# Performance work log

Hardware: AMD Instinct MI355X
Metric: run time of the kernel (lower is better)

## Reference

```python
import jax, jax.numpy as jnp
import numpy as np

EPS = 1e-7

def fake_quant(x, bits):
    """Per-tensor affine fake-quantization (dnn-gating TorchRoundToBits),
    matching torch.fake_quantize_per_tensor_affine with dynamic range."""
    fp_max = jax.lax.stop_gradient(jnp.max(x))
    fp_min = jax.lax.stop_gradient(jnp.min(x))
    qmax = float(2 ** bits - 1)
    qmin = 0.0
    scale = (fp_max - fp_min) / (qmax - qmin) + EPS
    zero_point = jnp.trunc(qmin - fp_min / scale)  # int() cast in torch truncates
    q = jnp.round(x / scale + zero_point)
    qc = jnp.clip(q, qmin, qmax)
    return (qc - zero_point) * scale

def conv2d(x, w, stride=1, padding=1):
    return jax.lax.conv_general_dilated(
        x, w,
        window_strides=(stride, stride),
        padding=[(padding, padding), (padding, padding)],
        dimension_numbers=('NCHW', 'OIHW', 'NCHW'))

def setup_inputs() -> dict:
    key = jax.random.key(0)
    k1, k2 = jax.random.split(key)
    x = jax.random.normal(k1, (32, 256, 56, 56), dtype=jnp.float32)
    # kaiming-like init for a 3x3 conv with 256 in-channels
    fan_in = 256 * 3 * 3
    weight = jax.random.normal(k2, (256, 256, 3, 3), dtype=jnp.float32) / np.sqrt(fan_in)
    return {"x": x, "weight": weight}

def reference(x, weight):
    WBITS, ABITS, PGABITS = 8, 8, 4
    TH = 0.99
    w_q = fake_quant(weight, WBITS)          # quantized weights (shared by both convs)
    msb_in = fake_quant(x, PGABITS)          # low-precision (MSB) input
    msb_out = conv2d(msb_in, w_q)            # [32,256,56,56] prediction pass
    lsb_in = fake_quant(x, ABITS) - msb_in   # residual (LSB) input
    lsb_out = conv2d(lsb_in, w_q)            # high-precision correction pass
    mask = (jax.nn.sigmoid(msb_out) > TH).astype(msb_out.dtype)
    return msb_out + mask * lsb_out
```

## Files before the change

kernel.cpp:

```cpp
#include <hip/hip_runtime.h>
#include <stdint.h>
#include <stddef.h>

typedef int v4i  __attribute__((ext_vector_type(4)));
typedef int v16i __attribute__((ext_vector_type(16)));

struct QParams {
  float s4, z4, s8, z8, sw, zw;
  float s4sw, s8sw;
  int dw;
};

__global__ void k_minmax2(const float4* __restrict__ x, int nx4,
                          const float4* __restrict__ w, int nw4,
                          float2* __restrict__ mmX, float2* __restrict__ mmW) {
  const float4* p; int n4; float2* slot; int base; int nblk;
  if (blockIdx.x < 1024) { p = x; n4 = nx4; slot = mmX + blockIdx.x;          base = blockIdx.x;        nblk = 1024; }
  else                   { p = w; n4 = nw4; slot = mmW + (blockIdx.x - 1024); base = blockIdx.x - 1024; nblk = 64; }
  float lmin = 3.4e38f, lmax = -3.4e38f;
  for (int i = base * blockDim.x + threadIdx.x; i < n4; i += nblk * blockDim.x) {
    float4 v = p[i];
    lmin = fminf(lmin, fminf(fminf(v.x, v.y), fminf(v.z, v.w)));
    lmax = fmaxf(lmax, fmaxf(fmaxf(v.x, v.y), fmaxf(v.z, v.w)));
  }
  for (int off = 32; off; off >>= 1) {
    lmin = fminf(lmin, __shfl_down(lmin, off, 64));
    lmax = fmaxf(lmax, __shfl_down(lmax, off, 64));
  }
  __shared__ float smin[4], smax[4];
  int w2 = threadIdx.x >> 6, lane = threadIdx.x & 63;
  if (lane == 0) { smin[w2] = lmin; smax[w2] = lmax; }
  __syncthreads();
  if (threadIdx.x == 0) {
    float2 r;
    r.x = fminf(fminf(smin[0], smin[1]), fminf(smin[2], smin[3]));
    r.y = fmaxf(fmaxf(smax[0], smax[1]), fmaxf(smax[2], smax[3]));
    *slot = r;
  }
}

__device__ __forceinline__ void quant2(float v, float s4, float z4, float s8, float z8,
                                       char& o4, char& o8) {
  float q4 = rintf(__fdiv_rn(v, s4) + z4);
  q4 = fminf(fmaxf(q4, 0.0f), 15.0f);
  o4 = (char)(int)(q4 - z4);
  float q8 = rintf(__fdiv_rn(v, s8) + z8);
  q8 = fminf(fmaxf(q8, 0.0f), 255.0f);
  int t8 = (int)(q8 - z8);
  o8 = (char)max(-128, min(127, t8));
}

__global__ void k_quant(const float4* __restrict__ x4, const float* __restrict__ wt,
                        const float2* __restrict__ mmX, const float2* __restrict__ mmW,
                        char* __restrict__ A4, char* __restrict__ A8,
                        int* __restrict__ CS4, int* __restrict__ CS8,
                        char* __restrict__ Wc,
                        QParams* __restrict__ prm, unsigned* __restrict__ zp) {
  __shared__ char sm4[56 * 260];
  __shared__ char sm8[56 * 260];
  __shared__ int cp4[56][4], cp8[56][4];
  __shared__ float s_red[4][4];
  __shared__ QParams sq;
  int tid = threadIdx.x;

  {
    float xmn = 3.4e38f, xmx = -3.4e38f, wmn = 3.4e38f, wmx = -3.4e38f;
#pragma unroll
    for (int i = 0; i < 4; ++i) {
      float2 v = mmX[i * 256 + tid];
      xmn = fminf(xmn, v.x); xmx = fmaxf(xmx, v.y);
    }
    if (tid < 64) { float2 v = mmW[tid]; wmn = v.x; wmx = v.y; }
    for (int off = 32; off; off >>= 1) {
      xmn = fminf(xmn, __shfl_down(xmn, off, 64));
      xmx = fmaxf(xmx, __shfl_down(xmx, off, 64));
      wmn = fminf(wmn, __shfl_down(wmn, off, 64));
      wmx = fmaxf(wmx, __shfl_down(wmx, off, 64));
    }
    int wv = tid >> 6, ln = tid & 63;
    if (ln == 0) { s_red[wv][0] = xmn; s_red[wv][1] = xmx; s_red[wv][2] = wmn; s_red[wv][3] = wmx; }
    __syncthreads();
    if (tid == 0) {
      float xmin = fminf(fminf(s_red[0][0], s_red[1][0]), fminf(s_red[2][0], s_red[3][0]));
      float xmax = fmaxf(fmaxf(s_red[0][1], s_red[1][1]), fmaxf(s_red[2][1], s_red[3][1]));
      float wmin = fminf(fminf(s_red[0][2], s_red[1][2]), fminf(s_red[2][2], s_red[3][2]));
      float wmax = fmaxf(fmaxf(s_red[0][3], s_red[1][3]), fmaxf(s_red[2][3], s_red[3][3]));
      float s4 = (xmax - xmin) / 15.0f + 1e-7f;
      sq.s4 = s4; sq.z4 = truncf(0.0f - xmin / s4);
      float s8 = (xmax - xmin) / 255.0f + 1e-7f;
      sq.s8 = s8; sq.z8 = truncf(0.0f - xmin / s8);
      float sw = (wmax - wmin) / 255.0f + 1e-7f;
      sq.sw = sw; sq.zw = truncf(0.0f - wmin / sw);
      sq.s4sw = s4 * sw; sq.s8sw = s8 * sw;
      sq.dw = 128 - (int)sq.zw;
    }
    __syncthreads();
  }

  if (blockIdx.x >= 1792) {
    int b = blockIdx.x - 1792;
    float sw = sq.sw, zw = sq.zw;
    char* smw = sm4;
    const float* src = wt + (size_t)b * 2304;
#pragma unroll
    for (int j = 0; j < 9; ++j) {
      int o = j * 256 + tid;
      float qf = rintf(__fdiv_rn(src[o], sw) + zw);
      qf = fminf(fmaxf(qf, 0.0f), 255.0f);
      int c = o / 9, jj = o - c * 9;
      smw[jj * 256 + c] = (char)((int)qf - 128);
    }
    __syncthreads();
    if (tid < 64) {
#pragma unroll
      for (int j = 0; j < 9; ++j)
        *(unsigned*)(Wc + (size_t)j * 65536 + b * 256 + tid * 4) =
            *(const unsigned*)(smw + j * 256 + tid * 4);
    }
    if (blockIdx.x == 1792) {
      if (tid < 128) zp[tid] = 0u;
      if (tid == 0) *prm = sq;
    }
    return;
  }

  int bx = blockIdx.x;
  int n = bx / 56, y = bx % 56;
  float s4 = sq.s4, z4 = sq.z4, s8 = sq.s8, z8 = sq.z8;
  const float4* xrow = x4 + (size_t)n * 200704 + y * 14;
#pragma unroll 2
  for (int it = 0; it < 14; ++it) {
    int idx = it * 256 + tid;
    int c = idx / 14, xq = idx - c * 14;
    float4 v = xrow[(size_t)c * 784 + xq];
    int b = (xq * 4) * 260 + c;
    char a0, b0; quant2(v.x, s4, z4, s8, z8, a0, b0);
    char a1, b1; quant2(v.y, s4, z4, s8, z8, a1, b1);
    char a2, b2; quant2(v.z, s4, z4, s8, z8, a2, b2);
    char a3, b3; quant2(v.w, s4, z4, s8, z8, a3, b3);
    sm4[b] = a0; sm4[b + 260] = a1; sm4[b + 520] = a2; sm4[b + 780] = a3;
    sm8[b] = b0; sm8[b + 260] = b1; sm8[b + 520] = b2; sm8[b + 780] = b3;
  }
  __syncthreads();
  if (tid < 224) {
    int xc = tid >> 2, qq = tid & 3;
    const unsigned* r4 = (const unsigned*)(sm4 + xc * 260 + qq * 64);
    const unsigned* r8 = (const unsigned*)(sm8 + xc * 260 + qq * 64);
    int a = 0, b = 0;
#pragma unroll
    for (int cw = 0; cw < 16; ++cw) {
      unsigned u = r4[cw], v = r8[cw];
      a += (int)(signed char)(u) + (int)(signed char)(u >> 8)
         + (int)(signed char)(u >> 16) + (int)(signed char)(u >> 24);
      b += (int)(signed char)(v) + (int)(signed char)(v >> 8)
         + (int)(signed char)(v >> 16) + (int)(signed char)(v >> 24);
    }
    cp4[xc][qq] = a; cp8[xc][qq] = b;
  }
  __syncthreads();
  int pixbase = n * 3136 + y * 56;
  if (tid < 56) {
    CS4[pixbase + tid] = cp4[tid][0] + cp4[tid][1] + cp4[tid][2] + cp4[tid][3];
    CS8[pixbase + tid] = cp8[tid][0] + cp8[tid][1] + cp8[tid][2] + cp8[tid][3];
  }
  unsigned* A4w = (unsigned*)A4;
  unsigned* A8w = (unsigned*)A8;
#pragma unroll 2
  for (int it = 0; it < 14; ++it) {
    int idx = it * 256 + tid;
    int xc = idx >> 6, wd = idx & 63;
    size_t o = (size_t)(pixbase + xc) * 64 + wd;
    A4w[o] = *(const unsigned*)(sm4 + xc * 260 + wd * 4);
    A8w[o] = *(const unsigned*)(sm8 + xc * 260 + wd * 4);
  }
}

__global__ void k_wsum(const int* __restrict__ CS4, const int* __restrict__ CS8,
                       int* __restrict__ S4, int* __restrict__ S8) {
  int p = blockIdx.x * 256 + threadIdx.x;
  if (p >= 100352) return;
  int rem = p % 3136;
  int y = rem / 56, xc = rem % 56;
  int a = 0, b = 0;
#pragma unroll
  for (int dy = -1; dy <= 1; ++dy) {
    if ((unsigned)(y + dy) >= 56u) continue;
#pragma unroll
    for (int dx = -1; dx <= 1; ++dx) {
      if ((unsigned)(xc + dx) >= 56u) continue;
      int qq = p + dy * 56 + dx;
      a += CS4[qq]; b += CS8[qq];
    }
  }
  S4[p] = a; S8[p] = b;
}

#define GLD16(gp, lp)                                                         \
  __builtin_amdgcn_global_load_lds((const __attribute__((address_space(1))) void*)(gp), \
                                   (__attribute__((address_space(3))) void*)(lp), 16, 0, 0)

__device__ __forceinline__ float pg_merge(int a4v, int a8v, float fs4, float fs8) {
  float msb = fs4 * (float)a4v;
  float c8  = fs8 * (float)a8v;
  float lsb = c8 - msb;
  float sig = 1.0f / (1.0f + expf(-msb));
  return msb + (sig > 0.99f ? lsb : 0.0f);
}

struct StagePtrs {
  const char* aBase0; const char* aBase1;
  const char* a8Base0; const char* a8Base1;
  const char* bBase0; const char* bBase1;
  const char* zp0;
  unsigned vm0, vm1;
};

__device__ __forceinline__ void issue_stage(int s, const StagePtrs& P,
                                            char* dA4, char* dA8, char* dB) {
  int win = s >> 2;
  int cs = (s & 3) << 6;
  int dy = win / 3 - 1;
  int dx = win - (dy + 1) * 3 - 1;
  int doff = (dy * 56 + dx) * 256 + cs;
  bool ok0 = (P.vm0 >> win) & 1;
  bool ok1 = (P.vm1 >> win) & 1;
  const char* g40 = ok0 ? P.aBase0 + doff : P.zp0;
  const char* g41 = ok1 ? P.aBase1 + doff : P.zp0;
  const char* g80 = ok0 ? P.a8Base0 + doff : P.zp0;
  const char* g81 = ok1 ? P.a8Base1 + doff : P.zp0;
  const char* gB0 = P.bBase0 + win * 65536 + cs;
  const char* gB1 = P.bBase1 + win * 65536 + cs;
  if (s >= 36) { gB0 = P.zp0; gB1 = P.zp0; }
  GLD16(g40, dA4);       GLD16(g41, dA4 + 1024);
  GLD16(g80, dA8);       GLD16(g81, dA8 + 1024);
  GLD16(gB0, dB);        GLD16(gB1, dB + 1024);
}

__global__ __launch_bounds__(256, 2) void k_conv(
    const char* __restrict__ A4, const char* __restrict__ A8,
    const char* __restrict__ Wc,
    const int* __restrict__ S4, const int* __restrict__ S8,
    const QParams* __restrict__ q, const char* __restrict__ zpage,
    float* __restrict__ out) {
  __shared__ char smA4[2][8192], smA8[2][8192], smB[2][8192];
  const size_t ASZ = 25690112;
  int tid = threadIdx.x;
  int w = tid >> 6, lane = tid & 63;

  int bid = blockIdx.x;
  int swz = (bid & 7) * 196 + (bid >> 3);
  int m0 = (swz >> 1) * 128;
  int n0 = (swz & 1) * 128;
  int wm = w >> 1, wn = w & 1;

  int chunk = lane & 3;
  int r0 = (w << 5) + (lane >> 2);
  int r1 = r0 + 16;
  int cg0 = chunk ^ ((r0 >> 1) & 3);
  int cg1 = chunk ^ ((r1 >> 1) & 3);
  int p0 = m0 + r0, p1 = m0 + r1;
  int rem0 = p0 % 3136, rem1 = p1 % 3136;
  int y0 = rem0 / 56, x0 = rem0 % 56;
  int y1 = rem1 / 56, x1 = rem1 % 56;

  StagePtrs P;
  P.aBase0 = A4 + (size_t)p0 * 256 + cg0 * 16;
  P.aBase1 = A4 + (size_t)p1 * 256 + cg1 * 16;
  P.a8Base0 = P.aBase0 + ASZ;
  P.a8Base1 = P.aBase1 + ASZ;
  P.bBase0 = Wc + (n0 + r0) * 256 + cg0 * 16;
  P.bBase1 = Wc + (n0 + r1) * 256 + cg1 * 16;
  P.zp0 = zpage + chunk * 16;
  P.vm0 = 0; P.vm1 = 0;
#pragma unroll
  for (int win = 0; win < 9; ++win) {
    int dy = win / 3 - 1, dx = win % 3 - 1;
    P.vm0 |= (unsigned)(((unsigned)(y0 + dy) < 56u) & ((unsigned)(x0 + dx) < 56u)) << win;
    P.vm1 |= (unsigned)(((unsigned)(y1 + dy) < 56u) & ((unsigned)(x1 + dx) < 56u)) << win;
  }

  char* dA4 = &smA4[0][w << 11];
  char* dA8 = &smA8[0][w << 11];
  char* dB  = &smB[0][w << 11];
  const char* smA4f = &smA4[0][0];
  const char* smA8f = &smA8[0][0];
  const char* smBf  = &smB[0][0];

  v16i acc4[2][2] = {}, acc8[2][2] = {};
  int r31 = lane & 31, qh = lane >> 5;

  int offA[2][2], offB[2][2];
#pragma unroll
  for (int fm = 0; fm < 2; ++fm) {
    int row = wm * 64 + fm * 32 + r31;
    int swl = (row >> 1) & 3;
#pragma unroll
    for (int kc = 0; kc < 2; ++kc)
      offA[fm][kc] = row * 64 + (((kc * 2 + qh) ^ swl) << 4);
  }
#pragma unroll
  for (int fn = 0; fn < 2; ++fn) {
    int row = wn * 64 + fn * 32 + r31;
    int swl = (row >> 1) & 3;
#pragma unroll
    for (int kc = 0; kc < 2; ++kc)
      offB[fn][kc] = row * 64 + (((kc * 2 + qh) ^ swl) << 4);
  }

#define STAGE(S, RB, WB)                                                      \
  {                                                                           \
    asm volatile("s_waitcnt vmcnt(0)" ::: "memory");                          \
    asm volatile("s_barrier" ::: "memory");                                   \
    issue_stage((S) + 1, P, dA4 + (WB) * 8192, dA8 + (WB) * 8192,             \
                dB + (WB) * 8192);                                            \
    __builtin_amdgcn_sched_barrier(0);       \
    _Pragma("unroll")                                                         \
    for (int kc = 0; kc < 2; ++kc) {                                          \
      v4i a4f[2], a8f[2], bf[2];                                              \
      _Pragma("unroll")                                                       \
      for (int fm = 0; fm < 2; ++fm) {                                        \
        a4f[fm] = *(const v4i*)(smA4f + (RB) * 8192 + offA[fm][kc]);          \
        a8f[fm] = *(const v4i*)(smA8f + (RB) * 8192 + offA[fm][kc]);          \
      }                                                                       \
      _Pragma("unroll")                                                       \
      for (int fn = 0; fn < 2; ++fn)                                          \
        bf[fn] = *(const v4i*)(smBf + (RB) * 8192 + offB[fn][kc]);            \
      __builtin_amdgcn_s_setprio(1);                                          \
      _Pragma("unroll")                                                       \
      for (int fm = 0; fm < 2; ++fm)                                          \
        _Pragma("unroll")                                                     \
        for (int fn = 0; fn < 2; ++fn) {                                      \
          acc4[fm][fn] = __builtin_amdgcn_mfma_i32_32x32x32_i8(a4f[fm], bf[fn], acc4[fm][fn], 0, 0, 0); \
          acc8[fm][fn] = __builtin_amdgcn_mfma_i32_32x32x32_i8(a8f[fm], bf[fn], acc8[fm][fn], 0, 0, 0); \
        }                                                                     \
      __builtin_amdgcn_s_setprio(0);                                          \
    }                                                                         \
  }

  issue_stage(0, P, dA4, dA8, dB);

#pragma unroll 1
  for (int sp = 0; sp < 18; ++sp) {
    int s0 = sp * 2;
    STAGE(s0,     0, 1);
    STAGE(s0 + 1, 1, 0);
  }
  asm volatile("s_waitcnt vmcnt(0)" ::: "memory");
#undef STAGE

  float fs4 = q->s4sw, fs8 = q->s8sw;
  int dwv = q->dw;
#pragma unroll
  for (int fm = 0; fm < 2; ++fm)
#pragma unroll
    for (int fn = 0; fn < 2; ++fn) {
      int kout = n0 + wn * 64 + fn * 32 + r31;
      int pb = m0 + wm * 64 + fm * 32 + 4 * qh;
#pragma unroll
      for (int rg = 0; rg < 4; ++rg) {
        int pr = pb + 8 * rg;
        int4 sv4 = *(const int4*)(S4 + pr);
        int4 sv8 = *(const int4*)(S8 + pr);
        float4 res;
        res.x = pg_merge(acc4[fm][fn][rg * 4 + 0] + dwv * sv4.x,
                         acc8[fm][fn][rg * 4 + 0] + dwv * sv8.x, fs4, fs8);
        res.y = pg_merge(acc4[fm][fn][rg * 4 + 1] + dwv * sv4.y,
                         acc8[fm][fn][rg * 4 + 1] + dwv * sv8.y, fs4, fs8);
        res.z = pg_merge(acc4[fm][fn][rg * 4 + 2] + dwv * sv4.z,
                         acc8[fm][fn][rg * 4 + 2] + dwv * sv8.z, fs4, fs8);
        res.w = pg_merge(acc4[fm][fn][rg * 4 + 3] + dwv * sv4.w,
                         acc8[fm][fn][rg * 4 + 3] + dwv * sv8.w, fs4, fs8);
        int nimg = pr / 3136;
        int rem = pr - nimg * 3136;
        *(float4*)(out + (size_t)nimg * 802816 + (size_t)kout * 3136 + rem) = res;
      }
    }
}

extern "C" void kernel_launch(void* const* d_in, const int* in_sizes, int n_in,
                              void* d_out, int out_size, void* d_ws, size_t ws_size,
                              hipStream_t stream) {
  const float* x  = (const float*)d_in[0];
  const float* wt = (const float*)d_in[1];
  float* out = (float*)d_out;

  char* ws = (char*)d_ws;
  float2* mmX = (float2*)ws;
  float2* mmW = (float2*)(ws + 8192);
  QParams* prm = (QParams*)(ws + 8960);
  char* zpage = ws + 9728;
  char* A4 = ws + 10240;
  const size_t ASZ = 25690112;
  char* A8 = A4 + ASZ;
  int* CS4 = (int*)(A8 + ASZ);
  int* CS8 = CS4 + 100352;
  int* S4  = CS8 + 100352;
  int* S8  = S4 + 100352;
  char* Wc = (char*)(S8 + 100352);

  k_minmax2<<<1088, 256, 0, stream>>>((const float4*)x, 25690112 / 4,
                                      (const float4*)wt, 589824 / 4, mmX, mmW);
  k_quant<<<2048, 256, 0, stream>>>((const float4*)x, wt, mmX, mmW,
                                    A4, A8, CS4, CS8, Wc, prm, (unsigned*)zpage);
  k_wsum<<<392, 256, 0, stream>>>(CS4, CS8, S4, S8);
  k_conv<<<dim3(1568), 256, 0, stream>>>(A4, A8, Wc, S4, S8, prm, zpage, out);
}
```

Before: 384.8 us.

## Split conv block into eight waves with 32x64 warp tiles

Doubles the conv workgroup from 256 to 512 threads, so each wave computes a 32x64 output sub-tile with two accumulator fragments per precision instead of four. Each wave now issues one async global-to-LDS load per operand per stage instead of two. The goal is more waves in flight to hide latency and less accumulator register pressure per wave. In exchange, fewer MFMAs run per LDS fragment read, and the tighter launch bound (512,4) may force spills, while the 48KB of LDS per block may cap residency below the requested four blocks.

Result: slower. 396.5 us (+3.0%).

```diff
diff --git a/kernel.cpp b/kernel.cpp
--- a/kernel.cpp
+++ b/kernel.cpp
@@ -208,11 +208,11 @@
 }
 
 struct StagePtrs {
-  const char* aBase0; const char* aBase1;
-  const char* a8Base0; const char* a8Base1;
-  const char* bBase0; const char* bBase1;
+  const char* aBase0;
+  const char* a8Base0;
+  const char* bBase0;
   const char* zp0;
-  unsigned vm0, vm1;
+  unsigned vm0;
 };
 
 __device__ __forceinline__ void issue_stage(int s, const StagePtrs& P,
@@ -223,20 +223,14 @@
   int dx = win - (dy + 1) * 3 - 1;
   int doff = (dy * 56 + dx) * 256 + cs;
   bool ok0 = (P.vm0 >> win) & 1;
-  bool ok1 = (P.vm1 >> win) & 1;
-  const char* g40 = ok0 ? P.aBase0 + doff : P.zp0;
-  const char* g41 = ok1 ? P.aBase1 + doff : P.zp0;
-  const char* g80 = ok0 ? P.a8Base0 + doff : P.zp0;
-  const char* g81 = ok1 ? P.a8Base1 + doff : P.zp0;
-  const char* gB0 = P.bBase0 + win * 65536 + cs;
-  const char* gB1 = P.bBase1 + win * 65536 + cs;
-  if (s >= 36) { gB0 = P.zp0; gB1 = P.zp0; }
-  GLD16(g40, dA4);       GLD16(g41, dA4 + 1024);
-  GLD16(g80, dA8);       GLD16(g81, dA8 + 1024);
-  GLD16(gB0, dB);        GLD16(gB1, dB + 1024);
-}
-
-__global__ __launch_bounds__(256, 2) void k_conv(
+  const char* g4 = ok0 ? P.aBase0 + doff : P.zp0;
+  const char* g8 = ok0 ? P.a8Base0 + doff : P.zp0;
+  const char* gB = P.bBase0 + win * 65536 + cs;
+  if (s >= 36) gB = P.zp0;
+  GLD16(g4, dA4); GLD16(g8, dA8); GLD16(gB, dB);
+}
+
+__global__ __launch_bounds__(512, 4) void k_conv(
     const char* __restrict__ A4, const char* __restrict__ A8,
     const char* __restrict__ Wc,
     const int* __restrict__ S4, const int* __restrict__ S8,
@@ -254,49 +248,41 @@
   int wm = w >> 1, wn = w & 1;
 
   int chunk = lane & 3;
-  int r0 = (w << 5) + (lane >> 2);
-  int r1 = r0 + 16;
+  int r0 = (w << 4) + (lane >> 2);
   int cg0 = chunk ^ ((r0 >> 1) & 3);
-  int cg1 = chunk ^ ((r1 >> 1) & 3);
-  int p0 = m0 + r0, p1 = m0 + r1;
-  int rem0 = p0 % 3136, rem1 = p1 % 3136;
+  int p0 = m0 + r0;
+  int rem0 = p0 % 3136;
   int y0 = rem0 / 56, x0 = rem0 % 56;
-  int y1 = rem1 / 56, x1 = rem1 % 56;
 
   StagePtrs P;
   P.aBase0 = A4 + (size_t)p0 * 256 + cg0 * 16;
-  P.aBase1 = A4 + (size_t)p1 * 256 + cg1 * 16;
   P.a8Base0 = P.aBase0 + ASZ;
-  P.a8Base1 = P.aBase1 + ASZ;
   P.bBase0 = Wc + (n0 + r0) * 256 + cg0 * 16;
-  P.bBase1 = Wc + (n0 + r1) * 256 + cg1 * 16;
   P.zp0 = zpage + chunk * 16;
-  P.vm0 = 0; P.vm1 = 0;
+  P.vm0 = 0;
 #pragma unroll
   for (int win = 0; win < 9; ++win) {
     int dy = win / 3 - 1, dx = win % 3 - 1;
     P.vm0 |= (unsigned)(((unsigned)(y0 + dy) < 56u) & ((unsigned)(x0 + dx) < 56u)) << win;
-    P.vm1 |= (unsigned)(((unsigned)(y1 + dy) < 56u) & ((unsigned)(x1 + dx) < 56u)) << win;
-  }
-
-  char* dA4 = &smA4[0][w << 11];
-  char* dA8 = &smA8[0][w << 11];
-  char* dB  = &smB[0][w << 11];
+  }
+
+  char* dA4 = &smA4[0][w << 10];
+  char* dA8 = &smA8[0][w << 10];
+  char* dB  = &smB[0][w << 10];
   const char* smA4f = &smA4[0][0];
   const char* smA8f = &smA8[0][0];
   const char* smBf  = &smB[0][0];
 
-  v16i acc4[2][2] = {}, acc8[2][2] = {};
+  v16i acc4[2] = {}, acc8[2] = {};
   int r31 = lane & 31, qh = lane >> 5;
 
-  int offA[2][2], offB[2][2];
-#pragma unroll
-  for (int fm = 0; fm < 2; ++fm) {
-    int row = wm * 64 + fm * 32 + r31;
+  int offA[2], offB[2][2];
+  {
+    int row = wm * 32 + r31;
     int swl = (row >> 1) & 3;
 #pragma unroll
     for (int kc = 0; kc < 2; ++kc)
-      offA[fm][kc] = row * 64 + (((kc * 2 + qh) ^ swl) << 4);
+      offA[kc] = row * 64 + (((kc * 2 + qh) ^ swl) << 4);
   }
 #pragma unroll
   for (int fn = 0; fn < 2; ++fn) {
@@ -316,23 +302,18 @@
     __builtin_amdgcn_sched_barrier(0);       \
     _Pragma("unroll")                                                         \
     for (int kc = 0; kc < 2; ++kc) {                                          \
-      v4i a4f[2], a8f[2], bf[2];                                              \
-      _Pragma("unroll")                                                       \
-      for (int fm = 0; fm < 2; ++fm) {                                        \
-        a4f[fm] = *(const v4i*)(smA4f + (RB) * 8192 + offA[fm][kc]);          \
-        a8f[fm] = *(const v4i*)(smA8f + (RB) * 8192 + offA[fm][kc]);          \
-      }                                                                       \
+      v4i a4f, a8f, bf[2];                                                    \
+      a4f = *(const v4i*)(smA4f + (RB) * 8192 + offA[kc]);                    \
+      a8f = *(const v4i*)(smA8f + (RB) * 8192 + offA[kc]);                    \
       _Pragma("unroll")                                                       \
       for (int fn = 0; fn < 2; ++fn)                                          \
         bf[fn] = *(const v4i*)(smBf + (RB) * 8192 + offB[fn][kc]);            \
       __builtin_amdgcn_s_setprio(1);                                          \
       _Pragma("unroll")                                                       \
-      for (int fm = 0; fm < 2; ++fm)                                          \
-        _Pragma("unroll")                                                     \
-        for (int fn = 0; fn < 2; ++fn) {                                      \
-          acc4[fm][fn] = __builtin_amdgcn_mfma_i32_32x32x32_i8(a4f[fm], bf[fn], acc4[fm][fn], 0, 0, 0); \
-          acc8[fm][fn] = __builtin_amdgcn_mfma_i32_32x32x32_i8(a8f[fm], bf[fn], acc8[fm][fn], 0, 0, 0); \
-        }                                                                     \
+      for (int fn = 0; fn < 2; ++fn) {                                        \
+        acc4[fn] = __builtin_amdgcn_mfma_i32_32x32x32_i8(a4f, bf[fn], acc4[fn], 0, 0, 0); \
+        acc8[fn] = __builtin_amdgcn_mfma_i32_32x32x32_i8(a8f, bf[fn], acc8[fn], 0, 0, 0); \
+      }                                                                       \
       __builtin_amdgcn_s_setprio(0);                                          \
     }                                                                         \
   }
@@ -351,30 +332,28 @@
   float fs4 = q->s4sw, fs8 = q->s8sw;
   int dwv = q->dw;
 #pragma unroll
-  for (int fm = 0; fm < 2; ++fm)
-#pragma unroll
-    for (int fn = 0; fn < 2; ++fn) {
-      int kout = n0 + wn * 64 + fn * 32 + r31;
-      int pb = m0 + wm * 64 + fm * 32 + 4 * qh;
-#pragma unroll
-      for (int rg = 0; rg < 4; ++rg) {
-        int pr = pb + 8 * rg;
-        int4 sv4 = *(const int4*)(S4 + pr);
-        int4 sv8 = *(const int4*)(S8 + pr);
-        float4 res;
-        res.x = pg_merge(acc4[fm][fn][rg * 4 + 0] + dwv * sv4.x,
-                         acc8[fm][fn][rg * 4 + 0] + dwv * sv8.x, fs4, fs8);
-        res.y = pg_merge(acc4[fm][fn][rg * 4 + 1] + dwv * sv4.y,
-                         acc8[fm][fn][rg * 4 + 1] + dwv * sv8.y, fs4, fs8);
-        res.z = pg_merge(acc4[fm][fn][rg * 4 + 2] + dwv * sv4.z,
-                         acc8[fm][fn][rg * 4 + 2] + dwv * sv8.z, fs4, fs8);
-        res.w = pg_merge(acc4[fm][fn][rg * 4 + 3] + dwv * sv4.w,
-                         acc8[fm][fn][rg * 4 + 3] + dwv * sv8.w, fs4, fs8);
-        int nimg = pr / 3136;
-        int rem = pr - nimg * 3136;
-        *(float4*)(out + (size_t)nimg * 802816 + (size_t)kout * 3136 + rem) = res;
-      }
-    }
+  for (int fn = 0; fn < 2; ++fn) {
+    int kout = n0 + wn * 64 + fn * 32 + r31;
+    int pb = m0 + wm * 32 + 4 * qh;
+#pragma unroll
+    for (int rg = 0; rg < 4; ++rg) {
+      int pr = pb + 8 * rg;
+      int4 sv4 = *(const int4*)(S4 + pr);
+      int4 sv8 = *(const int4*)(S8 + pr);
+      float4 res;
+      res.x = pg_merge(acc4[fn][rg * 4 + 0] + dwv * sv4.x,
+                       acc8[fn][rg * 4 + 0] + dwv * sv8.x, fs4, fs8);
+      res.y = pg_merge(acc4[fn][rg * 4 + 1] + dwv * sv4.y,
+                       acc8[fn][rg * 4 + 1] + dwv * sv8.y, fs4, fs8);
+      res.z = pg_merge(acc4[fn][rg * 4 + 2] + dwv * sv4.z,
+                       acc8[fn][rg * 4 + 2] + dwv * sv8.z, fs4, fs8);
+      res.w = pg_merge(acc4[fn][rg * 4 + 3] + dwv * sv4.w,
+                       acc8[fn][rg * 4 + 3] + dwv * sv8.w, fs4, fs8);
+      int nimg = pr / 3136;
+      int rem = pr - nimg * 3136;
+      *(float4*)(out + (size_t)nimg * 802816 + (size_t)kout * 3136 + rem) = res;
+    }
+  }
 }
 
 extern "C" void kernel_launch(void* const* d_in, const int* in_sizes, int n_in,
@@ -403,5 +382,5 @@
   k_quant<<<2048, 256, 0, stream>>>((const float4*)x, wt, mmX, mmW,
                                     A4, A8, CS4, CS8, Wc, prm, (unsigned*)zpage);
   k_wsum<<<392, 256, 0, stream>>>(CS4, CS8, S4, S8);
-  k_conv<<<dim3(1568), 256, 0, stream>>>(A4, A8, Wc, S4, S8, prm, zpage, out);
-}
+  k_conv<<<dim3(1568), 512, 0, stream>>>(A4, A8, Wc, S4, S8, prm, zpage, out);
+}
```
